# Performance work log

Measured on AMD Instinct MI355X. Metric: run time of the kernel, lower is better.

## Reference

```python
import jax, jax.numpy as jnp
import numpy as np

EPS = 1e-5

def layer_norm(x, g, b):
    mu = jnp.mean(x, axis=-1, keepdims=True)
    var = jnp.mean(jnp.square(x - mu), axis=-1, keepdims=True)
    return (x - mu) * jax.lax.rsqrt(var + EPS) * g + b

def setup_inputs() -> dict:
    key = jax.random.key(0)
    B, N, IN_D, S, D = 64, 4096, 256, 8, 256
    ks = jax.random.split(key, 20)
    scale = lambda fan_in: 1.0 / np.sqrt(fan_in)
    u = lambda k, shape, s: jax.random.uniform(k, shape, jnp.float32, -s, s)
    return {
        "inputs": jax.random.normal(ks[0], (B, N, IN_D), jnp.float32),
        "noise": jax.random.normal(ks[1], (B, S, D), jnp.float32),
        "slots_mu": jax.random.normal(ks[2], (1, S, D), jnp.float32),
        "slots_sigma": jnp.ones((1, S, D), jnp.float32) * 0.1,
        "Wq": u(ks[3], (D, D), scale(D)), "bq": u(ks[4], (D,), scale(D)),
        "Wk": u(ks[5], (D, IN_D), scale(IN_D)), "bk": u(ks[6], (D,), scale(IN_D)),
        "Wv": u(ks[7], (D, IN_D), scale(IN_D)), "bv": u(ks[8], (D,), scale(IN_D)),
        "W_ih": u(ks[9], (3 * D, D), scale(D)), "b_ih": u(ks[10], (3 * D,), scale(D)),
        "W_hh": u(ks[11], (3 * D, D), scale(D)), "b_hh": u(ks[12], (3 * D,), scale(D)),
        "W1": u(ks[13], (D, D), scale(D)), "b1": u(ks[14], (D,), scale(D)),
        "W2": u(ks[15], (D, D), scale(D)), "b2": u(ks[16], (D,), scale(D)),
        "ln_slots_g": jnp.ones((D,), jnp.float32), "ln_slots_b": jnp.zeros((D,), jnp.float32),
        "ln_mlp_g": jnp.ones((D,), jnp.float32), "ln_mlp_b": jnp.zeros((D,), jnp.float32),
    }

def gru_cell(x, h, W_ih, b_ih, W_hh, b_hh):
    # PyTorch GRUCell: gates ordered (reset, update, new)
    gi = x @ W_ih.T + b_ih  # [B*S, 3D]
    gh = h @ W_hh.T + b_hh
    i_r, i_z, i_n = jnp.split(gi, 3, axis=-1)
    h_r, h_z, h_n = jnp.split(gh, 3, axis=-1)
    r = jax.nn.sigmoid(i_r + h_r)
    z = jax.nn.sigmoid(i_z + h_z)
    n = jnp.tanh(i_n + r * h_n)
    return (1.0 - z) * n + z * h

def reference(inputs, noise, slots_mu, slots_sigma, Wq, bq, Wk, bk, Wv, bv,
              W_ih, b_ih, W_hh, b_hh, W1, b1, W2, b2,
              ln_slots_g, ln_slots_b, ln_mlp_g, ln_mlp_b):
    B, N, _ = inputs.shape
    _, S, D = noise.shape
    num_iterations = 3
    slots = slots_mu + slots_sigma * noise  # [B, S, D]
    # k, v are loop-invariant; hoist the big GEMMs out of the iteration loop
    k = jnp.einsum('bnd,ed->bne', inputs, Wk) + bk  # [B, N, D]
    v = jnp.einsum('bnd,ed->bne', inputs, Wv) + bv  # [B, N, D]
    inv_sqrt_d = 1.0 / np.sqrt(D)
    for _ in range(num_iterations):
        slots_prev = slots
        q = layer_norm(slots, ln_slots_g, ln_slots_b) @ Wq.T + bq  # [B, S, D]
        attn_logits = jnp.einsum('bsd,bnd->bsn', q, k) * inv_sqrt_d
        attn = jax.nn.softmax(attn_logits, axis=-1)  # softmax over inputs (dim=-1)
        updates = jnp.einsum('bsn,bnd->bsd', attn, v)  # [B, S, D]
        h_new = gru_cell(updates.reshape(-1, D), slots_prev.reshape(-1, D),
                         W_ih, b_ih, W_hh, b_hh).reshape(B, S, D)
        slots = slots_prev + h_new  # residual around GRU (as in source)
        hidden = jax.nn.relu(layer_norm(slots, ln_mlp_g, ln_mlp_b) @ W1.T + b1)
        slots = slots + (hidden @ W2.T + b2)
    return slots
```

## Files before the change

### kernel.cpp

```cpp
#include <hip/hip_runtime.h>


constexpr int Bn = 64;
constexpr int Nn = 4096;
constexpr int Dd = 256;
constexpr int Ss = 8;
constexpr int CH = 16;
constexpr float EPSF = 1e-5f;

#define DEV __device__ __forceinline__

using short8 = __attribute__((ext_vector_type(8))) short;
using f32x4 = __attribute__((ext_vector_type(4))) float;
union U8 { short8 s; uint4 u; };

DEV unsigned bfpack2(float lo, float hi) {
  unsigned ul = __float_as_uint(lo), uh = __float_as_uint(hi);
  ul = (ul + 0x7FFFu + ((ul >> 16) & 1u)) >> 16;
  uh = (uh + 0x7FFFu + ((uh >> 16) & 1u)) & 0xFFFF0000u;
  return ul | uh;
}
DEV unsigned short bf16r(float x) {
  unsigned u = __float_as_uint(x);
  u = (u + 0x7FFFu + ((u >> 16) & 1u)) >> 16;
  return (unsigned short)u;
}
DEV float rsum32(float v) {
  v += __shfl_xor(v, 1); v += __shfl_xor(v, 2); v += __shfl_xor(v, 4);
  v += __shfl_xor(v, 8); v += __shfl_xor(v, 16);
  return v;
}
DEV float sigm(float x) { return 1.f / (1.f + __expf(-x)); }

template <int NK>
DEV void load_af(short8* a, const unsigned short* base, int lda, int m16, int quad) {
  const unsigned short* p = base + m16 * lda + quad * 8;
#pragma unroll
  for (int kk = 0; kk < NK; ++kk) a[kk] = *(const short8*)(p + kk * 32);
}
template <int NK>
DEV f32x4 gemm_tile(const short8* a, const unsigned short* wr, float binit) {
  f32x4 acc = {binit, binit, binit, binit};
#pragma unroll
  for (int kk = 0; kk < NK; ++kk) {
    short8 b = *(const short8*)(wr + kk * 32);
    acc = __builtin_amdgcn_mfma_f32_16x16x32_bf16(a[kk], b, acc, 0, 0, 0);
  }
  return acc;
}

DEV void ln_row8(const float* x, const float* g, const float* b, int d0,
                 unsigned short* dst) {
  float s = x[0] + x[1] + x[2] + x[3] + x[4] + x[5] + x[6] + x[7];
  float mu = rsum32(s) * (1.f / 256.f);
  float q = 0.f;
#pragma unroll
  for (int j = 0; j < 8; ++j) { float d = x[j] - mu; q += d * d; }
  float rs = rsqrtf(rsum32(q) * (1.f / 256.f) + EPSF);
  float o[8];
#pragma unroll
  for (int j = 0; j < 8; ++j) o[j] = (x[j] - mu) * rs * g[d0 + j] + b[d0 + j];
  uint4 w;
  w.x = bfpack2(o[0], o[1]); w.y = bfpack2(o[2], o[3]);
  w.z = bfpack2(o[4], o[5]); w.w = bfpack2(o[6], o[7]);
  *(uint4*)dst = w;
}

__global__ __launch_bounds__(256) void k_wqk(const float* __restrict__ Wq,
                                             const float* __restrict__ Wk,
                                             const float* __restrict__ bq,
                                             unsigned short* __restrict__ Wqk_b,
                                             float* __restrict__ bqk) {
  int tid = threadIdx.x, c = blockIdx.x;
  if (c < 256) {
    float acc = 0.f;
    for (int e = 0; e < 256; ++e) acc += Wq[e * 256 + tid] * Wk[e * 256 + c];
    Wqk_b[c * 256 + tid] = bf16r(acc);
  } else {
    float acc = 0.f;
    for (int e = 0; e < 256; ++e) acc += bq[e] * Wk[e * 256 + tid];
    bqk[tid] = acc;
  }
}

__global__ __launch_bounds__(256) void k_conv(
    const float* __restrict__ Wv, const float* __restrict__ Wih,
    const float* __restrict__ Whh, const float* __restrict__ W1,
    const float* __restrict__ W2,
    const float* __restrict__ bih, const float* __restrict__ bhh,
    unsigned* Wv_b, unsigned* Wzr_b, unsigned* Win_b, unsigned* Whn_b,
    unsigned* W1_b, unsigned* W2_b, float* bzr) {
  if (blockIdx.x >= 1152) {
    int i = (blockIdx.x - 1152) * 256 + threadIdx.x;
    if (i < 512) bzr[i] = bih[i] + bhh[i];
    return;
  }
  int p = blockIdx.x * 256 + threadIdx.x;
  const float* src; unsigned* dst;
  if (p < 32768) { src = Wv + 2 * p; dst = Wv_b + p; }
  else if (p < 163840) {
    int q = p - 32768, row = q >> 8, col = (q & 255) * 2;
    src = (col < 256) ? (Wih + row * 256 + col) : (Whh + row * 256 + col - 256);
    dst = Wzr_b + q;
  }
  else if (p < 196608) { int q = p - 163840; src = Wih + 512 * 256 + 2 * q; dst = Win_b + q; }
  else if (p < 229376) { int q = p - 196608; src = Whh + 512 * 256 + 2 * q; dst = Whn_b + q; }
  else if (p < 262144) { int q = p - 229376; src = W1 + 2 * q; dst = W1_b + q; }
  else { int q = p - 262144; src = W2 + 2 * q; dst = W2_b + q; }
  dst[0] = bfpack2(src[0], src[1]);
}

__global__ __launch_bounds__(512) void k_qk0(const float* __restrict__ noise,
                                             const float* __restrict__ s_mu,
                                             const float* __restrict__ s_sg,
                                             const float* __restrict__ gsl,
                                             const float* __restrict__ bsl,
                                             const unsigned short* __restrict__ Wqk_b,
                                             const float* __restrict__ bqk,
                                             float* __restrict__ slots,
                                             float* __restrict__ qk) {
  __shared__ __align__(16) unsigned short lnb[16 * 264];
  const int tid = threadIdx.x, bb = blockIdx.x;
  const int lane = tid & 63, wave = tid >> 6;
  const int m16 = lane & 15, quad = lane >> 4;
  const int row = tid >> 5, l32 = tid & 31, d0 = l32 * 8;
  {
    const int grow = bb * 16 + row;
    const int sidx = (grow & 7) * 256 + d0;
    const float* np = noise + (size_t)grow * 256 + d0;
    float4 n0 = *(const float4*)np, n1 = *(const float4*)(np + 4);
    float4 m0 = *(const float4*)(s_mu + sidx), m1 = *(const float4*)(s_mu + sidx + 4);
    float4 g0 = *(const float4*)(s_sg + sidx), g1 = *(const float4*)(s_sg + sidx + 4);
    float x[8] = {m0.x + g0.x * n0.x, m0.y + g0.y * n0.y,
                  m0.z + g0.z * n0.z, m0.w + g0.w * n0.w,
                  m1.x + g1.x * n1.x, m1.y + g1.y * n1.y,
                  m1.z + g1.z * n1.z, m1.w + g1.w * n1.w};
    float* sp_ = slots + (size_t)grow * 256 + d0;
    float4 o0, o1;
    o0.x = x[0]; o0.y = x[1]; o0.z = x[2]; o0.w = x[3];
    o1.x = x[4]; o1.y = x[5]; o1.z = x[6]; o1.w = x[7];
    *(float4*)sp_ = o0; *(float4*)(sp_ + 4) = o1;
    ln_row8(x, gsl, bsl, d0, lnb + row * 264 + d0);
  }
  __syncthreads();
  short8 a8[8];
  load_af<8>(a8, lnb, 264, m16, quad);
#pragma unroll
  for (int i = 0; i < 2; ++i) {
    int t = wave + 8 * i;
    f32x4 acc = gemm_tile<8>(a8, Wqk_b + (size_t)(t * 16 + m16) * 256 + quad * 8,
                             bqk[t * 16 + m16]);
#pragma unroll
    for (int r = 0; r < 4; ++r)
      qk[(size_t)(bb * 16 + quad * 4 + r) * 256 + t * 16 + m16] = acc[r] * 0.0625f;
  }
}

template <bool FIRST>
DEV void ld_chunk(const float* __restrict__ xin, unsigned* __restrict__ xbf,
                  size_t nbase, int tid, uint4* pr) {
#pragma unroll
  for (int i = 0; i < 8; ++i) {
    int flat = i * 256 + tid, n = flat >> 5, od = flat & 31;
    if (FIRST) {
      const float4* src = (const float4*)(xin + (nbase + n) * 256 + od * 8);
      float4 v0 = src[0], v1 = src[1];
      uint4 o;
      o.x = bfpack2(v0.x, v0.y); o.y = bfpack2(v0.z, v0.w);
      o.z = bfpack2(v1.x, v1.y); o.w = bfpack2(v1.z, v1.w);
      ((uint4*)xbf)[(nbase + n) * 32 + od] = o;
      pr[i] = o;
    } else {
      pr[i] = ((const uint4*)xbf)[(nbase + n) * 32 + od];
    }
  }
}

template <bool FIRST>
__global__ __launch_bounds__(256) void k_attn(const float* __restrict__ xin,
                                              unsigned* __restrict__ xbf,
                                              const float* __restrict__ qk,
                                              float* __restrict__ pl,
                                              float* __restrict__ pu) {
  __shared__ __align__(16) unsigned xt[128 * 65];
  __shared__ __align__(16) unsigned pp[32 * 17];
  __shared__ __align__(16) float lred[4][16];
  const int tid = threadIdx.x;
  const int lane = tid & 63, wave = tid >> 6;
  const int m16 = lane & 15, quad = lane >> 4;
  const int c = blockIdx.x, b = blockIdx.y;
  const int pb = (b * CH + c) * 8;
  const unsigned psel = (m16 & 1) ? 0x07060302u : 0x05040100u;

  short8 aq[8];
  {
    const float* qrow = qk + (size_t)(b * 8 + (m16 & 7)) * 256 + quad * 8;
#pragma unroll
    for (int kk = 0; kk < 8; ++kk) {
      U8 f;
      float4 q0 = *(const float4*)(qrow + kk * 32);
      float4 q1 = *(const float4*)(qrow + kk * 32 + 4);
      f.u.x = bfpack2(q0.x, q0.y); f.u.y = bfpack2(q0.z, q0.w);
      f.u.z = bfpack2(q1.x, q1.y); f.u.w = bfpack2(q1.z, q1.w);
      if (m16 >= 8) { f.u.x = 0u; f.u.y = 0u; f.u.z = 0u; f.u.w = 0u; }
      aq[kk] = f.s;
    }
  }
  float lacc[4] = {0.f, 0.f, 0.f, 0.f};
  f32x4 acc[4];
#pragma unroll
  for (int t = 0; t < 4; ++t) acc[t] = (f32x4){0.f, 0.f, 0.f, 0.f};
  const int d0w = wave * 64;

  uint4 pr[8];
  const size_t nb0 = (size_t)b * Nn + (size_t)c * 256;
  ld_chunk<FIRST>(xin, xbf, nb0, tid, pr);

  for (int ch = 0; ch < 4; ++ch) {
#pragma unroll
    for (int i = 0; i < 8; ++i) {
      int flat = i * 256 + tid, n = flat >> 5, od = flat & 31, rb = od * 4;
      xt[(rb + 0) * 65 + n] = pr[i].x;
      xt[(rb + 1) * 65 + n] = pr[i].y;
      xt[(rb + 2) * 65 + n] = pr[i].z;
      xt[(rb + 3) * 65 + n] = pr[i].w;
    }
    __syncthreads();
    if (ch + 1 < 4)
      ld_chunk<FIRST>(xin, xbf, nb0 + (size_t)(ch + 1) * 64, tid, pr);
    {
      const int nt = wave;
      f32x4 pacc = (f32x4){0.f, 0.f, 0.f, 0.f};
#pragma unroll
      for (int kk = 0; kk < 8; ++kk) {
        int base = (kk * 16 + quad * 4) * 65 + nt * 16 + m16;
        U8 bf;
        bf.u.x = xt[base]; bf.u.y = xt[base + 65];
        bf.u.z = xt[base + 130]; bf.u.w = xt[base + 195];
        pacc = __builtin_amdgcn_mfma_f32_16x16x32_bf16(aq[kk], bf.s, pacc, 0, 0, 0);
      }
      const int xrow = nt * 16 + m16;
      unsigned short* pps = (unsigned short*)pp;
#pragma unroll
      for (int r = 0; r < 4; ++r) {
        float p = __expf(pacc[r]);
        lacc[r] += p;
        pps[((xrow >> 1) * 17 + quad * 4 + r) * 2 + (xrow & 1)] = bf16r(p);
      }
    }
    __syncthreads();
#pragma unroll
    for (int nh = 0; nh < 2; ++nh) {
      U8 bp;
      bp.u.x = pp[(nh * 16 + quad * 4 + 0) * 17 + m16];
      bp.u.y = pp[(nh * 16 + quad * 4 + 1) * 17 + m16];
      bp.u.z = pp[(nh * 16 + quad * 4 + 2) * 17 + m16];
      bp.u.w = pp[(nh * 16 + quad * 4 + 3) * 17 + m16];
#pragma unroll
      for (int t = 0; t < 4; ++t) {
        int d = d0w + t * 16 + m16;
        const unsigned* xr = xt + (d >> 1) * 65 + nh * 32 + quad * 8;
        unsigned u0 = xr[0], u1 = xr[1], u2 = xr[2], u3 = xr[3];
        unsigned u4 = xr[4], u5 = xr[5], u6 = xr[6], u7 = xr[7];
        U8 af;
        af.u.x = __builtin_amdgcn_perm(u1, u0, psel);
        af.u.y = __builtin_amdgcn_perm(u3, u2, psel);
        af.u.z = __builtin_amdgcn_perm(u5, u4, psel);
        af.u.w = __builtin_amdgcn_perm(u7, u6, psel);
        acc[t] = __builtin_amdgcn_mfma_f32_16x16x32_bf16(af.s, bp.s, acc[t], 0, 0, 0);
      }
    }
    __syncthreads();
  }
  if (m16 < 8) {
#pragma unroll
    for (int t = 0; t < 4; ++t)
#pragma unroll
      for (int r = 0; r < 4; ++r)
        pu[(size_t)(pb + m16) * 256 + d0w + t * 16 + quad * 4 + r] = acc[t][r];
  }
  {
#pragma unroll
    for (int r = 0; r < 4; ++r) {
      float v = lacc[r];
      v += __shfl_xor(v, 1); v += __shfl_xor(v, 2);
      v += __shfl_xor(v, 4); v += __shfl_xor(v, 8);
      if (m16 == 0) lred[wave][quad * 4 + r] = v;
    }
  }
  __syncthreads();
  if (tid < 8)
    pl[pb + tid] = lred[0][tid] + lred[1][tid] + lred[2][tid] + lred[3][tid];
}

__global__ __launch_bounds__(512) void k_upd(
    const float* __restrict__ pl, const float* __restrict__ pu,
    const unsigned short* __restrict__ Wv_b, const float* __restrict__ bv,
    const unsigned short* __restrict__ Wzr_b, const float* __restrict__ bzr,
    const unsigned short* __restrict__ Win_b, const float* __restrict__ bin,
    const unsigned short* __restrict__ Whn_b, const float* __restrict__ bhn,
    const unsigned short* __restrict__ W1_b, const float* __restrict__ b1,
    const unsigned short* __restrict__ W2_b, const float* __restrict__ b2,
    const float* __restrict__ gml, const float* __restrict__ bml,
    const float* __restrict__ gsl, const float* __restrict__ bsl,
    const unsigned short* __restrict__ Wqk_b, const float* __restrict__ bqk,
    float* __restrict__ slots, float* __restrict__ qk, float* __restrict__ dout) {
  __shared__ __align__(16) unsigned short cat[16 * 520];
  __shared__ __align__(16) float sp[16 * 260];
  __shared__ __align__(16) float s1[16 * 260];
  __shared__ __align__(16) unsigned short lnb[16 * 264];
  const int tid = threadIdx.x, bb = blockIdx.x;
  const int lane = tid & 63, wave = tid >> 6;
  const int m16 = lane & 15, quad = lane >> 4;
  const int row = tid >> 5, l32 = tid & 31, d0 = l32 * 8;
  const int bat = 2 * bb + (row >> 3), sl = row & 7;
  {
    float L = 0.f;
#pragma unroll
    for (int cc = 0; cc < 16; ++cc) L += pl[(bat * 16 + cc) * 8 + sl];
    float li = 1.f / L;
    float a[8] = {0.f, 0.f, 0.f, 0.f, 0.f, 0.f, 0.f, 0.f};
    for (int cc = 0; cc < 16; ++cc) {
      const float* pp_ = pu + ((size_t)(bat * 16 + cc) * 8 + sl) * 256 + d0;
      float4 v0 = *(const float4*)pp_, v1 = *(const float4*)(pp_ + 4);
      a[0] += v0.x; a[1] += v0.y; a[2] += v0.z; a[3] += v0.w;
      a[4] += v1.x; a[5] += v1.y; a[6] += v1.z; a[7] += v1.w;
    }
    uint4 o;
    o.x = bfpack2(a[0] * li, a[1] * li); o.y = bfpack2(a[2] * li, a[3] * li);
    o.z = bfpack2(a[4] * li, a[5] * li); o.w = bfpack2(a[6] * li, a[7] * li);
    *(uint4*)(cat + row * 520 + d0) = o;
    const float* sp_ = slots + (size_t)(bb * 16 + row) * 256 + d0;
    float4 h0 = *(const float4*)sp_, h1 = *(const float4*)(sp_ + 4);
    *(float4*)(sp + row * 260 + d0) = h0;
    *(float4*)(sp + row * 260 + d0 + 4) = h1;
    uint4 hb;
    hb.x = bfpack2(h0.x, h0.y); hb.y = bfpack2(h0.z, h0.w);
    hb.z = bfpack2(h1.x, h1.y); hb.w = bfpack2(h1.z, h1.w);
    *(uint4*)(cat + row * 520 + 256 + d0) = hb;
  }
  __syncthreads();
  short8 afr[16];
  load_af<8>(afr, cat, 520, m16, quad);
  f32x4 accv[2];
#pragma unroll
  for (int i = 0; i < 2; ++i) {
    int t = wave + 8 * i;
    accv[i] = gemm_tile<8>(afr, Wv_b + (size_t)(t * 16 + m16) * 256 + quad * 8,
                           bv[t * 16 + m16]);
  }
  __syncthreads();
#pragma unroll
  for (int i = 0; i < 2; ++i) {
    int t = wave + 8 * i;
#pragma unroll
    for (int r = 0; r < 4; ++r)
      cat[(quad * 4 + r) * 520 + t * 16 + m16] = bf16r(accv[i][r]);
  }
  __syncthreads();
  load_af<16>(afr, cat, 520, m16, quad);
  f32x4 rr[2], zz[2];
#pragma unroll
  for (int i = 0; i < 2; ++i) {
    int t = wave + 8 * i;
    f32x4 ar = gemm_tile<16>(afr, Wzr_b + (size_t)(t * 16 + m16) * 512 + quad * 8,
                             bzr[t * 16 + m16]);
    f32x4 az = gemm_tile<16>(afr, Wzr_b + (size_t)((t + 16) * 16 + m16) * 512 + quad * 8,
                             bzr[(t + 16) * 16 + m16]);
#pragma unroll
    for (int r = 0; r < 4; ++r) { rr[i][r] = sigm(ar[r]); zz[i][r] = sigm(az[r]); }
  }
#pragma unroll
  for (int i = 0; i < 2; ++i) {
    int t = wave + 8 * i, col = t * 16 + m16;
    f32x4 ain = gemm_tile<8>(afr, Win_b + (size_t)(t * 16 + m16) * 256 + quad * 8,
                             bin[col]);
    f32x4 ahn = gemm_tile<8>(afr + 8, Whn_b + (size_t)(t * 16 + m16) * 256 + quad * 8,
                             bhn[col]);
#pragma unroll
    for (int r = 0; r < 4; ++r) {
      int rw = quad * 4 + r;
      float nin = ain[r] + rr[i][r] * ahn[r];
      float nn = 1.f - 2.f / (__expf(2.f * nin) + 1.f);
      float hpc = sp[rw * 260 + col];
      s1[rw * 260 + col] = hpc + (1.f - zz[i][r]) * nn + zz[i][r] * hpc;
    }
  }
  __syncthreads();
  {
    const float* s1r = s1 + row * 260 + d0;
    float4 v0 = *(const float4*)s1r, v1 = *(const float4*)(s1r + 4);
    float x[8] = {v0.x, v0.y, v0.z, v0.w, v1.x, v1.y, v1.z, v1.w};
    ln_row8(x, gml, bml, d0, lnb + row * 264 + d0);
  }
  __syncthreads();
  load_af<8>(afr, lnb, 264, m16, quad);
#pragma unroll
  for (int i = 0; i < 2; ++i) {
    int t = wave + 8 * i;
    f32x4 acc = gemm_tile<8>(afr, W1_b + (size_t)(t * 16 + m16) * 256 + quad * 8,
                             b1[t * 16 + m16]);
#pragma unroll
    for (int r = 0; r < 4; ++r)
      cat[(quad * 4 + r) * 520 + t * 16 + m16] = bf16r(fmaxf(acc[r], 0.f));
  }
  __syncthreads();
  load_af<8>(afr, cat, 520, m16, quad);
#pragma unroll
  for (int i = 0; i < 2; ++i) {
    int t = wave + 8 * i;
    f32x4 acc = gemm_tile<8>(afr, W2_b + (size_t)(t * 16 + m16) * 256 + quad * 8,
                             b2[t * 16 + m16]);
#pragma unroll
    for (int r = 0; r < 4; ++r) {
      int rw = quad * 4 + r, col = t * 16 + m16;
      float v = acc[r] + s1[rw * 260 + col];
      size_t gi = (size_t)(bb * 16 + rw) * 256 + col;
      slots[gi] = v;
      if (dout) dout[gi] = v;
      sp[rw * 260 + col] = v;
    }
  }
  __syncthreads();
  {
    const float* spr = sp + row * 260 + d0;
    float4 v0 = *(const float4*)spr, v1 = *(const float4*)(spr + 4);
    float x[8] = {v0.x, v0.y, v0.z, v0.w, v1.x, v1.y, v1.z, v1.w};
    ln_row8(x, gsl, bsl, d0, lnb + row * 264 + d0);
  }
  __syncthreads();
  load_af<8>(afr, lnb, 264, m16, quad);
#pragma unroll
  for (int i = 0; i < 2; ++i) {
    int t = wave + 8 * i;
    f32x4 acc = gemm_tile<8>(afr, Wqk_b + (size_t)(t * 16 + m16) * 256 + quad * 8,
                             bqk[t * 16 + m16]);
#pragma unroll
    for (int r = 0; r < 4; ++r)
      qk[(size_t)(bb * 16 + quad * 4 + r) * 256 + t * 16 + m16] = acc[r] * 0.0625f;
  }
}

extern "C" void kernel_launch(void* const* d_in, const int* in_sizes, int n_in,
                              void* d_out, int out_size, void* d_ws, size_t ws_size,
                              hipStream_t stream) {
  const float* inputs = (const float*)d_in[0];
  const float* noise = (const float*)d_in[1];
  const float* s_mu = (const float*)d_in[2];
  const float* s_sg = (const float*)d_in[3];
  const float* Wq = (const float*)d_in[4];
  const float* bq = (const float*)d_in[5];
  const float* Wk = (const float*)d_in[6];
  const float* Wv = (const float*)d_in[8];
  const float* bv = (const float*)d_in[9];
  const float* Wih = (const float*)d_in[10];
  const float* bih = (const float*)d_in[11];
  const float* Whh = (const float*)d_in[12];
  const float* bhh = (const float*)d_in[13];
  const float* W1 = (const float*)d_in[14];
  const float* b1 = (const float*)d_in[15];
  const float* W2 = (const float*)d_in[16];
  const float* b2 = (const float*)d_in[17];
  const float* gsl = (const float*)d_in[18];
  const float* bsl = (const float*)d_in[19];
  const float* gml = (const float*)d_in[20];
  const float* bml = (const float*)d_in[21];
  float* out = (float*)d_out;

  char* wsb = (char*)d_ws;
  unsigned* xbf = (unsigned*)wsb;
  float* fp = (float*)(wsb + (size_t)Bn * Nn * Dd * 2);
  float* slots = fp; fp += Bn * Ss * Dd;
  float* qk = fp;    fp += Bn * Ss * Dd;
  float* bqk = fp;   fp += Dd;
  float* pl = fp;    fp += Bn * CH * Ss;
  float* pu = fp;    fp += Bn * CH * Ss * Dd;
  float* bzr = fp;   fp += 512;
  unsigned short* wb = (unsigned short*)fp;
  unsigned short* Wv_b = wb;  wb += 65536;
  unsigned short* Wzr_b = wb; wb += 262144;
  unsigned short* Win_b = wb; wb += 65536;
  unsigned short* Whn_b = wb; wb += 65536;
  unsigned short* W1_b = wb;  wb += 65536;
  unsigned short* W2_b = wb;  wb += 65536;
  unsigned short* Wqk_b = wb; wb += 65536;
  (void)in_sizes; (void)n_in; (void)out_size; (void)ws_size;

  k_wqk<<<dim3(257), dim3(256), 0, stream>>>(Wq, Wk, bq, Wqk_b, bqk);
  k_conv<<<dim3(1154), dim3(256), 0, stream>>>(
      Wv, Wih, Whh, W1, W2, bih, bhh, (unsigned*)Wv_b, (unsigned*)Wzr_b,
      (unsigned*)Win_b, (unsigned*)Whn_b, (unsigned*)W1_b, (unsigned*)W2_b, bzr);
  k_qk0<<<dim3(32), dim3(512), 0, stream>>>(noise, s_mu, s_sg, gsl, bsl, Wqk_b, bqk,
                                            slots, qk);
  for (int it = 0; it < 3; ++it) {
    if (it == 0)
      k_attn<true><<<dim3(CH, Bn), dim3(256), 0, stream>>>(inputs, xbf, qk, pl, pu);
    else
      k_attn<false><<<dim3(CH, Bn), dim3(256), 0, stream>>>(nullptr, xbf, qk, pl, pu);
    k_upd<<<dim3(32), dim3(512), 0, stream>>>(
        pl, pu, Wv_b, bv, Wzr_b, bzr, Win_b, bih + 512, Whn_b, bhh + 512, W1_b, b1,
        W2_b, b2, gml, bml, gsl, bsl, Wqk_b, bqk, slots, qk, (it == 2) ? out : nullptr);
  }
}
```

Measured before the change: 686.5 us.

## Fuse slot update into attention kernel via last-block atomic counter

Merges the two weight-prep kernels into one launch, and folds the per-iteration slot-update kernel into the attention kernel. Each attention block increments a per-batch-pair atomic counter, and the last of the 32 blocks for that pair runs the GRU/MLP/query update with 256 threads. This removes three kernel launches and their boundaries, but the update now runs serialized on a single straggler block per pair with half the threads, and it adds fences and atomics.

```diff
diff --git a/kernel.cpp b/kernel.cpp
--- a/kernel.cpp
+++ b/kernel.cpp
@@ -66,48 +66,333 @@
   *(uint4*)dst = w;
 }
 
-__global__ __launch_bounds__(256) void k_wqk(const float* __restrict__ Wq,
-                                             const float* __restrict__ Wk,
-                                             const float* __restrict__ bq,
-                                             unsigned short* __restrict__ Wqk_b,
-                                             float* __restrict__ bqk) {
-  int tid = threadIdx.x, c = blockIdx.x;
-  if (c < 256) {
+
+template <bool FIRST>
+DEV void ld_chunk_t(const float* __restrict__ xin, unsigned* __restrict__ xbf,
+                    size_t nbase, int tid, uint4* pr) {
+#pragma unroll
+  for (int i = 0; i < 8; ++i) {
+    int flat = i * 256 + tid, n = flat >> 5, od = flat & 31;
+    if (FIRST) {
+      const float4* src = (const float4*)(xin + (nbase + n) * 256 + od * 8);
+      float4 v0 = src[0], v1 = src[1];
+      uint4 o;
+      o.x = bfpack2(v0.x, v0.y); o.y = bfpack2(v0.z, v0.w);
+      o.z = bfpack2(v1.x, v1.y); o.w = bfpack2(v1.z, v1.w);
+      ((uint4*)xbf)[(nbase + n) * 32 + od] = o;
+      pr[i] = o;
+    } else {
+      pr[i] = ((const uint4*)xbf)[(nbase + n) * 32 + od];
+    }
+  }
+}
+
+template <bool FIRST>
+DEV void attn_unit(const float* __restrict__ xin, unsigned* __restrict__ xbf,
+                   const float* __restrict__ qk, float* __restrict__ pl,
+                   float* __restrict__ pu, unsigned* xt, unsigned* pp,
+                   float (*lred)[16], int u, int tid) {
+  const int lane = tid & 63, wave = tid >> 6;
+  const int m16 = lane & 15, quad = lane >> 4;
+  const int b = u >> 4, c = u & 15;
+  const int pb = u * 8;
+  const unsigned psel = (m16 & 1) ? 0x07060302u : 0x05040100u;
+
+  short8 aq[8];
+  {
+    const float* qrow = qk + (size_t)(b * 8 + (m16 & 7)) * 256 + quad * 8;
+#pragma unroll
+    for (int kk = 0; kk < 8; ++kk) {
+      U8 f;
+      float4 q0 = *(const float4*)(qrow + kk * 32);
+      float4 q1 = *(const float4*)(qrow + kk * 32 + 4);
+      f.u.x = bfpack2(q0.x, q0.y); f.u.y = bfpack2(q0.z, q0.w);
+      f.u.z = bfpack2(q1.x, q1.y); f.u.w = bfpack2(q1.z, q1.w);
+      if (m16 >= 8) { f.u.x = 0u; f.u.y = 0u; f.u.z = 0u; f.u.w = 0u; }
+      aq[kk] = f.s;
+    }
+  }
+  float lacc[4] = {0.f, 0.f, 0.f, 0.f};
+  f32x4 acc[4];
+#pragma unroll
+  for (int t = 0; t < 4; ++t) acc[t] = (f32x4){0.f, 0.f, 0.f, 0.f};
+  const int d0w = wave * 64;
+
+  uint4 pr[8];
+  const size_t nb0 = (size_t)b * Nn + (size_t)c * 256;
+  ld_chunk_t<FIRST>(xin, xbf, nb0, tid, pr);
+
+  for (int ch = 0; ch < 4; ++ch) {
+#pragma unroll
+    for (int i = 0; i < 8; ++i) {
+      int flat = i * 256 + tid, n = flat >> 5, od = flat & 31, rb = od * 4;
+      xt[(rb + 0) * 65 + n] = pr[i].x;
+      xt[(rb + 1) * 65 + n] = pr[i].y;
+      xt[(rb + 2) * 65 + n] = pr[i].z;
+      xt[(rb + 3) * 65 + n] = pr[i].w;
+    }
+    __syncthreads();
+    if (ch + 1 < 4)
+      ld_chunk_t<FIRST>(xin, xbf, nb0 + (size_t)(ch + 1) * 64, tid, pr);
+    {
+      const int nt = wave;
+      f32x4 pacc = (f32x4){0.f, 0.f, 0.f, 0.f};
+#pragma unroll
+      for (int kk = 0; kk < 8; ++kk) {
+        int base = (kk * 16 + quad * 4) * 65 + nt * 16 + m16;
+        U8 bf;
+        bf.u.x = xt[base]; bf.u.y = xt[base + 65];
+        bf.u.z = xt[base + 130]; bf.u.w = xt[base + 195];
+        pacc = __builtin_amdgcn_mfma_f32_16x16x32_bf16(aq[kk], bf.s, pacc, 0, 0, 0);
+      }
+      const int xrow = nt * 16 + m16;
+      unsigned short* pps = (unsigned short*)pp;
+#pragma unroll
+      for (int r = 0; r < 4; ++r) {
+        float p = __expf(pacc[r]);
+        lacc[r] += p;
+        pps[((xrow >> 1) * 17 + quad * 4 + r) * 2 + (xrow & 1)] = bf16r(p);
+      }
+    }
+    __syncthreads();
+#pragma unroll
+    for (int nh = 0; nh < 2; ++nh) {
+      U8 bp;
+      bp.u.x = pp[(nh * 16 + quad * 4 + 0) * 17 + m16];
+      bp.u.y = pp[(nh * 16 + quad * 4 + 1) * 17 + m16];
+      bp.u.z = pp[(nh * 16 + quad * 4 + 2) * 17 + m16];
+      bp.u.w = pp[(nh * 16 + quad * 4 + 3) * 17 + m16];
+#pragma unroll
+      for (int t = 0; t < 4; ++t) {
+        int d = d0w + t * 16 + m16;
+        const unsigned* xr = xt + (d >> 1) * 65 + nh * 32 + quad * 8;
+        unsigned u0 = xr[0], u1 = xr[1], u2 = xr[2], u3 = xr[3];
+        unsigned u4 = xr[4], u5 = xr[5], u6 = xr[6], u7 = xr[7];
+        U8 af;
+        af.u.x = __builtin_amdgcn_perm(u1, u0, psel);
+        af.u.y = __builtin_amdgcn_perm(u3, u2, psel);
+        af.u.z = __builtin_amdgcn_perm(u5, u4, psel);
+        af.u.w = __builtin_amdgcn_perm(u7, u6, psel);
+        acc[t] = __builtin_amdgcn_mfma_f32_16x16x32_bf16(af.s, bp.s, acc[t], 0, 0, 0);
+      }
+    }
+    __syncthreads();
+  }
+  if (m16 < 8) {
+#pragma unroll
+    for (int t = 0; t < 4; ++t)
+#pragma unroll
+      for (int r = 0; r < 4; ++r)
+        pu[(size_t)(pb + m16) * 256 + d0w + t * 16 + quad * 4 + r] = acc[t][r];
+  }
+#pragma unroll
+  for (int r = 0; r < 4; ++r) {
+    float v = lacc[r];
+    v += __shfl_xor(v, 1); v += __shfl_xor(v, 2);
+    v += __shfl_xor(v, 4); v += __shfl_xor(v, 8);
+    if (m16 == 0) lred[wave][quad * 4 + r] = v;
+  }
+  __syncthreads();
+  if (tid < 8)
+    pl[pb + tid] = lred[0][tid] + lred[1][tid] + lred[2][tid] + lred[3][tid];
+}
+
+DEV void upd_body256(
+    const float* __restrict__ pl, const float* __restrict__ pu,
+    const unsigned short* __restrict__ Wv_b, const float* __restrict__ bv,
+    const unsigned short* __restrict__ Wzr_b, const float* __restrict__ bzr,
+    const unsigned short* __restrict__ Win_b, const float* __restrict__ bin,
+    const unsigned short* __restrict__ Whn_b, const float* __restrict__ bhn,
+    const unsigned short* __restrict__ W1_b, const float* __restrict__ b1,
+    const unsigned short* __restrict__ W2_b, const float* __restrict__ b2,
+    const float* __restrict__ gml, const float* __restrict__ bml,
+    const float* __restrict__ gsl, const float* __restrict__ bsl,
+    const unsigned short* __restrict__ Wqk_b, const float* __restrict__ bqk,
+    float* __restrict__ slots, float* __restrict__ qk, float* __restrict__ dout,
+    unsigned short* cat, float* sp, int bb, int tid) {
+  unsigned short* lnbp = cat + 256;
+  const int lane = tid & 63, wave4 = tid >> 6;
+  const int m16 = lane & 15, quad = lane >> 4;
+  const int row8 = tid >> 5, l32 = tid & 31, d0 = l32 * 8;
+#pragma unroll
+  for (int r2 = 0; r2 < 2; ++r2) {
+    const int row = row8 + 8 * r2;
+    const int bat = 2 * bb + (row >> 3), sl = row & 7;
+    float L = 0.f;
+#pragma unroll
+    for (int cc = 0; cc < 16; ++cc) L += pl[(bat * 16 + cc) * 8 + sl];
+    float li = 1.f / L;
+    float a[8] = {0.f, 0.f, 0.f, 0.f, 0.f, 0.f, 0.f, 0.f};
+    for (int cc = 0; cc < 16; ++cc) {
+      const float* pp_ = pu + ((size_t)(bat * 16 + cc) * 8 + sl) * 256 + d0;
+      float4 v0 = *(const float4*)pp_, v1 = *(const float4*)(pp_ + 4);
+      a[0] += v0.x; a[1] += v0.y; a[2] += v0.z; a[3] += v0.w;
+      a[4] += v1.x; a[5] += v1.y; a[6] += v1.z; a[7] += v1.w;
+    }
+    uint4 o;
+    o.x = bfpack2(a[0] * li, a[1] * li); o.y = bfpack2(a[2] * li, a[3] * li);
+    o.z = bfpack2(a[4] * li, a[5] * li); o.w = bfpack2(a[6] * li, a[7] * li);
+    *(uint4*)(cat + row * 520 + d0) = o;
+    const float* sp_ = slots + (size_t)(bb * 16 + row) * 256 + d0;
+    float4 h0 = *(const float4*)sp_, h1 = *(const float4*)(sp_ + 4);
+    *(float4*)(sp + row * 260 + d0) = h0;
+    *(float4*)(sp + row * 260 + d0 + 4) = h1;
+    uint4 hb;
+    hb.x = bfpack2(h0.x, h0.y); hb.y = bfpack2(h0.z, h0.w);
+    hb.z = bfpack2(h1.x, h1.y); hb.w = bfpack2(h1.z, h1.w);
+    *(uint4*)(cat + row * 520 + 256 + d0) = hb;
+  }
+  __syncthreads();
+  short8 afr[16];
+  load_af<8>(afr, cat, 520, m16, quad);
+  f32x4 accv[4];
+#pragma unroll
+  for (int i = 0; i < 4; ++i) {
+    int t = wave4 + 4 * i;
+    accv[i] = gemm_tile<8>(afr, Wv_b + (size_t)(t * 16 + m16) * 256 + quad * 8,
+                           bv[t * 16 + m16]);
+  }
+  __syncthreads();
+#pragma unroll
+  for (int i = 0; i < 4; ++i) {
+    int t = wave4 + 4 * i;
+#pragma unroll
+    for (int r = 0; r < 4; ++r)
+      cat[(quad * 4 + r) * 520 + t * 16 + m16] = bf16r(accv[i][r]);
+  }
+  __syncthreads();
+  load_af<16>(afr, cat, 520, m16, quad);
+#pragma unroll
+  for (int i = 0; i < 4; ++i) {
+    int t = wave4 + 4 * i, col = t * 16 + m16;
+    f32x4 ar = gemm_tile<16>(afr, Wzr_b + (size_t)(t * 16 + m16) * 512 + quad * 8,
+                             bzr[t * 16 + m16]);
+    f32x4 az = gemm_tile<16>(afr, Wzr_b + (size_t)((t + 16) * 16 + m16) * 512 + quad * 8,
+                             bzr[(t + 16) * 16 + m16]);
+    f32x4 ain = gemm_tile<8>(afr, Win_b + (size_t)(t * 16 + m16) * 256 + quad * 8,
+                             bin[col]);
+    f32x4 ahn = gemm_tile<8>(afr + 8, Whn_b + (size_t)(t * 16 + m16) * 256 + quad * 8,
+                             bhn[col]);
+#pragma unroll
+    for (int r = 0; r < 4; ++r) {
+      int rw = quad * 4 + r;
+      float rrv = sigm(ar[r]), zzv = sigm(az[r]);
+      float nin = ain[r] + rrv * ahn[r];
+      float nn = 1.f - 2.f / (__expf(2.f * nin) + 1.f);
+      float hpc = sp[rw * 260 + col];
+      sp[rw * 260 + col] = hpc + (1.f - zzv) * nn + zzv * hpc;
+    }
+  }
+  __syncthreads();
+#pragma unroll
+  for (int r2 = 0; r2 < 2; ++r2) {
+    int row = row8 + 8 * r2;
+    const float* s1r = sp + row * 260 + d0;
+    float4 v0 = *(const float4*)s1r, v1 = *(const float4*)(s1r + 4);
+    float x[8] = {v0.x, v0.y, v0.z, v0.w, v1.x, v1.y, v1.z, v1.w};
+    ln_row8(x, gml, bml, d0, lnbp + row * 520 + d0);
+  }
+  __syncthreads();
+  load_af<8>(afr, lnbp, 520, m16, quad);
+#pragma unroll
+  for (int i = 0; i < 4; ++i) {
+    int t = wave4 + 4 * i;
+    f32x4 acc = gemm_tile<8>(afr, W1_b + (size_t)(t * 16 + m16) * 256 + quad * 8,
+                             b1[t * 16 + m16]);
+#pragma unroll
+    for (int r = 0; r < 4; ++r)
+      cat[(quad * 4 + r) * 520 + t * 16 + m16] = bf16r(fmaxf(acc[r], 0.f));
+  }
+  __syncthreads();
+  load_af<8>(afr, cat, 520, m16, quad);
+#pragma unroll
+  for (int i = 0; i < 4; ++i) {
+    int t = wave4 + 4 * i;
+    f32x4 acc = gemm_tile<8>(afr, W2_b + (size_t)(t * 16 + m16) * 256 + quad * 8,
+                             b2[t * 16 + m16]);
+#pragma unroll
+    for (int r = 0; r < 4; ++r) {
+      int rw = quad * 4 + r, col = t * 16 + m16;
+      float v = acc[r] + sp[rw * 260 + col];
+      size_t gi = (size_t)(bb * 16 + rw) * 256 + col;
+      slots[gi] = v;
+      if (dout) dout[gi] = v;
+      sp[rw * 260 + col] = v;
+    }
+  }
+  __syncthreads();
+#pragma unroll
+  for (int r2 = 0; r2 < 2; ++r2) {
+    int row = row8 + 8 * r2;
+    const float* spr = sp + row * 260 + d0;
+    float4 v0 = *(const float4*)spr, v1 = *(const float4*)(spr + 4);
+    float x[8] = {v0.x, v0.y, v0.z, v0.w, v1.x, v1.y, v1.z, v1.w};
+    ln_row8(x, gsl, bsl, d0, lnbp + row * 520 + d0);
+  }
+  __syncthreads();
+  load_af<8>(afr, lnbp, 520, m16, quad);
+#pragma unroll
+  for (int i = 0; i < 4; ++i) {
+    int t = wave4 + 4 * i;
+    f32x4 acc = gemm_tile<8>(afr, Wqk_b + (size_t)(t * 16 + m16) * 256 + quad * 8,
+                             bqk[t * 16 + m16]);
+#pragma unroll
+    for (int r = 0; r < 4; ++r)
+      qk[(size_t)(bb * 16 + quad * 4 + r) * 256 + t * 16 + m16] = acc[r] * 0.0625f;
+  }
+}
+
+DEV void prep_unit(int u, int tid,
+                   const float* Wq, const float* Wk, const float* bq,
+                   unsigned short* Wqk_b, float* bqk,
+                   const float* Wv, const float* Wih, const float* Whh,
+                   const float* W1, const float* W2,
+                   const float* bih, const float* bhh,
+                   unsigned* Wv_b, unsigned* Wzr_b, unsigned* Win_b, unsigned* Whn_b,
+                   unsigned* W1_b, unsigned* W2_b, float* bzr) {
+  if (u < 256) {
     float acc = 0.f;
-    for (int e = 0; e < 256; ++e) acc += Wq[e * 256 + tid] * Wk[e * 256 + c];
-    Wqk_b[c * 256 + tid] = bf16r(acc);
-  } else {
+    for (int e = 0; e < 256; ++e) acc += Wq[e * 256 + tid] * Wk[e * 256 + u];
+    Wqk_b[u * 256 + tid] = bf16r(acc);
+  } else if (u == 256) {
     float acc = 0.f;
     for (int e = 0; e < 256; ++e) acc += bq[e] * Wk[e * 256 + tid];
     bqk[tid] = acc;
-  }
-}
-
-__global__ __launch_bounds__(256) void k_conv(
-    const float* __restrict__ Wv, const float* __restrict__ Wih,
-    const float* __restrict__ Whh, const float* __restrict__ W1,
-    const float* __restrict__ W2,
+  } else {
+    int cu = u - 257;
+    if (cu >= 1152) {
+      int i = (cu - 1152) * 256 + tid;
+      if (i < 512) bzr[i] = bih[i] + bhh[i];
+      return;
+    }
+    int p = cu * 256 + tid;
+    const float* src; unsigned* dst;
+    if (p < 32768) { src = Wv + 2 * p; dst = Wv_b + p; }
+    else if (p < 163840) {
+      int q = p - 32768, row = q >> 8, col = (q & 255) * 2;
+      src = (col < 256) ? (Wih + row * 256 + col) : (Whh + row * 256 + col - 256);
+      dst = Wzr_b + q;
+    }
+    else if (p < 196608) { int q = p - 163840; src = Wih + 512 * 256 + 2 * q; dst = Win_b + q; }
+    else if (p < 229376) { int q = p - 196608; src = Whh + 512 * 256 + 2 * q; dst = Whn_b + q; }
+    else if (p < 262144) { int q = p - 229376; src = W1 + 2 * q; dst = W1_b + q; }
+    else { int q = p - 262144; src = W2 + 2 * q; dst = W2_b + q; }
+    dst[0] = bfpack2(src[0], src[1]);
+  }
+}
+
+
+__global__ __launch_bounds__(256) void k_prep(
+    const float* __restrict__ Wq, const float* __restrict__ Wk,
+    const float* __restrict__ bq, unsigned short* __restrict__ Wqk_b,
+    float* __restrict__ bqk, const float* __restrict__ Wv,
+    const float* __restrict__ Wih, const float* __restrict__ Whh,
+    const float* __restrict__ W1, const float* __restrict__ W2,
     const float* __restrict__ bih, const float* __restrict__ bhh,
     unsigned* Wv_b, unsigned* Wzr_b, unsigned* Win_b, unsigned* Whn_b,
     unsigned* W1_b, unsigned* W2_b, float* bzr) {
-  if (blockIdx.x >= 1152) {
-    int i = (blockIdx.x - 1152) * 256 + threadIdx.x;
-    if (i < 512) bzr[i] = bih[i] + bhh[i];
-    return;
-  }
-  int p = blockIdx.x * 256 + threadIdx.x;
-  const float* src; unsigned* dst;
-  if (p < 32768) { src = Wv + 2 * p; dst = Wv_b + p; }
-  else if (p < 163840) {
-    int q = p - 32768, row = q >> 8, col = (q & 255) * 2;
-    src = (col < 256) ? (Wih + row * 256 + col) : (Whh + row * 256 + col - 256);
-    dst = Wzr_b + q;
-  }
-  else if (p < 196608) { int q = p - 163840; src = Wih + 512 * 256 + 2 * q; dst = Win_b + q; }
-  else if (p < 229376) { int q = p - 196608; src = Whh + 512 * 256 + 2 * q; dst = Whn_b + q; }
-  else if (p < 262144) { int q = p - 229376; src = W1 + 2 * q; dst = W1_b + q; }
-  else { int q = p - 262144; src = W2 + 2 * q; dst = W2_b + q; }
-  dst[0] = bfpack2(src[0], src[1]);
+  prep_unit(blockIdx.x, threadIdx.x, Wq, Wk, bq, Wqk_b, bqk, Wv, Wih, Whh, W1, W2,
+            bih, bhh, Wv_b, Wzr_b, Win_b, Whn_b, W1_b, W2_b, bzr);
 }
 
 __global__ __launch_bounds__(512) void k_qk0(const float* __restrict__ noise,
@@ -118,9 +403,11 @@
                                              const unsigned short* __restrict__ Wqk_b,
                                              const float* __restrict__ bqk,
                                              float* __restrict__ slots,
-                                             float* __restrict__ qk) {
+                                             float* __restrict__ qk,
+                                             int* __restrict__ cnt) {
   __shared__ __align__(16) unsigned short lnb[16 * 264];
   const int tid = threadIdx.x, bb = blockIdx.x;
+  if (bb == 0 && tid < 32) cnt[tid] = 0;
   const int lane = tid & 63, wave = tid >> 6;
   const int m16 = lane & 15, quad = lane >> 4;
   const int row = tid >> 5, l32 = tid & 31, d0 = l32 * 8;
@@ -156,288 +443,42 @@
   }
 }
 
-template <bool FIRST>
-DEV void ld_chunk(const float* __restrict__ xin, unsigned* __restrict__ xbf,
-                  size_t nbase, int tid, uint4* pr) {
-#pragma unroll
-  for (int i = 0; i < 8; ++i) {
-    int flat = i * 256 + tid, n = flat >> 5, od = flat & 31;
-    if (FIRST) {
-      const float4* src = (const float4*)(xin + (nbase + n) * 256 + od * 8);
-      float4 v0 = src[0], v1 = src[1];
-      uint4 o;
-      o.x = bfpack2(v0.x, v0.y); o.y = bfpack2(v0.z, v0.w);
-      o.z = bfpack2(v1.x, v1.y); o.w = bfpack2(v1.z, v1.w);
-      ((uint4*)xbf)[(nbase + n) * 32 + od] = o;
-      pr[i] = o;
-    } else {
-      pr[i] = ((const uint4*)xbf)[(nbase + n) * 32 + od];
-    }
-  }
-}
-
-template <bool FIRST>
-__global__ __launch_bounds__(256) void k_attn(const float* __restrict__ xin,
-                                              unsigned* __restrict__ xbf,
-                                              const float* __restrict__ qk,
-                                              float* __restrict__ pl,
-                                              float* __restrict__ pu) {
-  __shared__ __align__(16) unsigned xt[128 * 65];
-  __shared__ __align__(16) unsigned pp[32 * 17];
-  __shared__ __align__(16) float lred[4][16];
+struct IterArgs {
+  const float* xin;
+  unsigned* xbf;
+  float *qk, *pl, *pu;
+  int* cnt;
+  const unsigned short *Wv_b, *Wzr_b, *Win_b, *Whn_b, *W1_b, *W2_b, *Wqk_b;
+  const float *bv, *bzr, *bin, *bhn, *b1, *b2, *gml, *bml, *gsl, *bsl, *bqk;
+  float *slots, *out;
+};
+
+template <int IT>
+__global__ __launch_bounds__(256) void k_attn_f(IterArgs a) {
+  __shared__ __align__(16) union SMU {
+    struct { unsigned xt[128 * 65]; unsigned pp[32 * 17]; float lred[4][16]; } at;
+    struct { unsigned short cat[16 * 520]; float sp[16 * 260]; } up;
+  } sm;
+  __shared__ int win;
   const int tid = threadIdx.x;
-  const int lane = tid & 63, wave = tid >> 6;
-  const int m16 = lane & 15, quad = lane >> 4;
-  const int c = blockIdx.x, b = blockIdx.y;
-  const int pb = (b * CH + c) * 8;
-  const unsigned psel = (m16 & 1) ? 0x07060302u : 0x05040100u;
-
-  short8 aq[8];
-  {
-    const float* qrow = qk + (size_t)(b * 8 + (m16 & 7)) * 256 + quad * 8;
-#pragma unroll
-    for (int kk = 0; kk < 8; ++kk) {
-      U8 f;
-      float4 q0 = *(const float4*)(qrow + kk * 32);
-      float4 q1 = *(const float4*)(qrow + kk * 32 + 4);
-      f.u.x = bfpack2(q0.x, q0.y); f.u.y = bfpack2(q0.z, q0.w);
-      f.u.z = bfpack2(q1.x, q1.y); f.u.w = bfpack2(q1.z, q1.w);
-      if (m16 >= 8) { f.u.x = 0u; f.u.y = 0u; f.u.z = 0u; f.u.w = 0u; }
-      aq[kk] = f.s;
-    }
-  }
-  float lacc[4] = {0.f, 0.f, 0.f, 0.f};
-  f32x4 acc[4];
-#pragma unroll
-  for (int t = 0; t < 4; ++t) acc[t] = (f32x4){0.f, 0.f, 0.f, 0.f};
-  const int d0w = wave * 64;
-
-  uint4 pr[8];
-  const size_t nb0 = (size_t)b * Nn + (size_t)c * 256;
-  ld_chunk<FIRST>(xin, xbf, nb0, tid, pr);
-
-  for (int ch = 0; ch < 4; ++ch) {
-#pragma unroll
-    for (int i = 0; i < 8; ++i) {
-      int flat = i * 256 + tid, n = flat >> 5, od = flat & 31, rb = od * 4;
-      xt[(rb + 0) * 65 + n] = pr[i].x;
-      xt[(rb + 1) * 65 + n] = pr[i].y;
-      xt[(rb + 2) * 65 + n] = pr[i].z;
-      xt[(rb + 3) * 65 + n] = pr[i].w;
-    }
-    __syncthreads();
-    if (ch + 1 < 4)
-      ld_chunk<FIRST>(xin, xbf, nb0 + (size_t)(ch + 1) * 64, tid, pr);
-    {
-      const int nt = wave;
-      f32x4 pacc = (f32x4){0.f, 0.f, 0.f, 0.f};
-#pragma unroll
-      for (int kk = 0; kk < 8; ++kk) {
-        int base = (kk * 16 + quad * 4) * 65 + nt * 16 + m16;
-        U8 bf;
-        bf.u.x = xt[base]; bf.u.y = xt[base + 65];
-        bf.u.z = xt[base + 130]; bf.u.w = xt[base + 195];
-        pacc = __builtin_amdgcn_mfma_f32_16x16x32_bf16(aq[kk], bf.s, pacc, 0, 0, 0);
-      }
-      const int xrow = nt * 16 + m16;
-      unsigned short* pps = (unsigned short*)pp;
-#pragma unroll
-      for (int r = 0; r < 4; ++r) {
-        float p = __expf(pacc[r]);
-        lacc[r] += p;
-        pps[((xrow >> 1) * 17 + quad * 4 + r) * 2 + (xrow & 1)] = bf16r(p);
-      }
-    }
-    __syncthreads();
-#pragma unroll
-    for (int nh = 0; nh < 2; ++nh) {
-      U8 bp;
-      bp.u.x = pp[(nh * 16 + quad * 4 + 0) * 17 + m16];
-      bp.u.y = pp[(nh * 16 + quad * 4 + 1) * 17 + m16];
-      bp.u.z = pp[(nh * 16 + quad * 4 + 2) * 17 + m16];
-      bp.u.w = pp[(nh * 16 + quad * 4 + 3) * 17 + m16];
-#pragma unroll
-      for (int t = 0; t < 4; ++t) {
-        int d = d0w + t * 16 + m16;
-        const unsigned* xr = xt + (d >> 1) * 65 + nh * 32 + quad * 8;
-        unsigned u0 = xr[0], u1 = xr[1], u2 = xr[2], u3 = xr[3];
-        unsigned u4 = xr[4], u5 = xr[5], u6 = xr[6], u7 = xr[7];
-        U8 af;
-        af.u.x = __builtin_amdgcn_perm(u1, u0, psel);
-        af.u.y = __builtin_amdgcn_perm(u3, u2, psel);
-        af.u.z = __builtin_amdgcn_perm(u5, u4, psel);
-        af.u.w = __builtin_amdgcn_perm(u7, u6, psel);
-        acc[t] = __builtin_amdgcn_mfma_f32_16x16x32_bf16(af.s, bp.s, acc[t], 0, 0, 0);
-      }
-    }
-    __syncthreads();
-  }
-  if (m16 < 8) {
-#pragma unroll
-    for (int t = 0; t < 4; ++t)
-#pragma unroll
-      for (int r = 0; r < 4; ++r)
-        pu[(size_t)(pb + m16) * 256 + d0w + t * 16 + quad * 4 + r] = acc[t][r];
-  }
-  {
-#pragma unroll
-    for (int r = 0; r < 4; ++r) {
-      float v = lacc[r];
-      v += __shfl_xor(v, 1); v += __shfl_xor(v, 2);
-      v += __shfl_xor(v, 4); v += __shfl_xor(v, 8);
-      if (m16 == 0) lred[wave][quad * 4 + r] = v;
-    }
-  }
-  __syncthreads();
-  if (tid < 8)
-    pl[pb + tid] = lred[0][tid] + lred[1][tid] + lred[2][tid] + lred[3][tid];
-}
-
-__global__ __launch_bounds__(512) void k_upd(
-    const float* __restrict__ pl, const float* __restrict__ pu,
-    const unsigned short* __restrict__ Wv_b, const float* __restrict__ bv,
-    const unsigned short* __restrict__ Wzr_b, const float* __restrict__ bzr,
-    const unsigned short* __restrict__ Win_b, const float* __restrict__ bin,
-    const unsigned short* __restrict__ Whn_b, const float* __restrict__ bhn,
-    const unsigned short* __restrict__ W1_b, const float* __restrict__ b1,
-    const unsigned short* __restrict__ W2_b, const float* __restrict__ b2,
-    const float* __restrict__ gml, const float* __restrict__ bml,
-    const float* __restrict__ gsl, const float* __restrict__ bsl,
-    const unsigned short* __restrict__ Wqk_b, const float* __restrict__ bqk,
-    float* __restrict__ slots, float* __restrict__ qk, float* __restrict__ dout) {
-  __shared__ __align__(16) unsigned short cat[16 * 520];
-  __shared__ __align__(16) float sp[16 * 260];
-  __shared__ __align__(16) float s1[16 * 260];
-  __shared__ __align__(16) unsigned short lnb[16 * 264];
-  const int tid = threadIdx.x, bb = blockIdx.x;
-  const int lane = tid & 63, wave = tid >> 6;
-  const int m16 = lane & 15, quad = lane >> 4;
-  const int row = tid >> 5, l32 = tid & 31, d0 = l32 * 8;
-  const int bat = 2 * bb + (row >> 3), sl = row & 7;
-  {
-    float L = 0.f;
-#pragma unroll
-    for (int cc = 0; cc < 16; ++cc) L += pl[(bat * 16 + cc) * 8 + sl];
-    float li = 1.f / L;
-    float a[8] = {0.f, 0.f, 0.f, 0.f, 0.f, 0.f, 0.f, 0.f};
-    for (int cc = 0; cc < 16; ++cc) {
-      const float* pp_ = pu + ((size_t)(bat * 16 + cc) * 8 + sl) * 256 + d0;
-      float4 v0 = *(const float4*)pp_, v1 = *(const float4*)(pp_ + 4);
-      a[0] += v0.x; a[1] += v0.y; a[2] += v0.z; a[3] += v0.w;
-      a[4] += v1.x; a[5] += v1.y; a[6] += v1.z; a[7] += v1.w;
-    }
-    uint4 o;
-    o.x = bfpack2(a[0] * li, a[1] * li); o.y = bfpack2(a[2] * li, a[3] * li);
-    o.z = bfpack2(a[4] * li, a[5] * li); o.w = bfpack2(a[6] * li, a[7] * li);
-    *(uint4*)(cat + row * 520 + d0) = o;
-    const float* sp_ = slots + (size_t)(bb * 16 + row) * 256 + d0;
-    float4 h0 = *(const float4*)sp_, h1 = *(const float4*)(sp_ + 4);
-    *(float4*)(sp + row * 260 + d0) = h0;
-    *(float4*)(sp + row * 260 + d0 + 4) = h1;
-    uint4 hb;
-    hb.x = bfpack2(h0.x, h0.y); hb.y = bfpack2(h0.z, h0.w);
-    hb.z = bfpack2(h1.x, h1.y); hb.w = bfpack2(h1.z, h1.w);
-    *(uint4*)(cat + row * 520 + 256 + d0) = hb;
-  }
-  __syncthreads();
-  short8 afr[16];
-  load_af<8>(afr, cat, 520, m16, quad);
-  f32x4 accv[2];
-#pragma unroll
-  for (int i = 0; i < 2; ++i) {
-    int t = wave + 8 * i;
-    accv[i] = gemm_tile<8>(afr, Wv_b + (size_t)(t * 16 + m16) * 256 + quad * 8,
-                           bv[t * 16 + m16]);
-  }
-  __syncthreads();
-#pragma unroll
-  for (int i = 0; i < 2; ++i) {
-    int t = wave + 8 * i;
-#pragma unroll
-    for (int r = 0; r < 4; ++r)
-      cat[(quad * 4 + r) * 520 + t * 16 + m16] = bf16r(accv[i][r]);
-  }
-  __syncthreads();
-  load_af<16>(afr, cat, 520, m16, quad);
-  f32x4 rr[2], zz[2];
-#pragma unroll
-  for (int i = 0; i < 2; ++i) {
-    int t = wave + 8 * i;
-    f32x4 ar = gemm_tile<16>(afr, Wzr_b + (size_t)(t * 16 + m16) * 512 + quad * 8,
-                             bzr[t * 16 + m16]);
-    f32x4 az = gemm_tile<16>(afr, Wzr_b + (size_t)((t + 16) * 16 + m16) * 512 + quad * 8,
-                             bzr[(t + 16) * 16 + m16]);
-#pragma unroll
-    for (int r = 0; r < 4; ++r) { rr[i][r] = sigm(ar[r]); zz[i][r] = sigm(az[r]); }
-  }
-#pragma unroll
-  for (int i = 0; i < 2; ++i) {
-    int t = wave + 8 * i, col = t * 16 + m16;
-    f32x4 ain = gemm_tile<8>(afr, Win_b + (size_t)(t * 16 + m16) * 256 + quad * 8,
-                             bin[col]);
-    f32x4 ahn = gemm_tile<8>(afr + 8, Whn_b + (size_t)(t * 16 + m16) * 256 + quad * 8,
-                             bhn[col]);
-#pragma unroll
-    for (int r = 0; r < 4; ++r) {
-      int rw = quad * 4 + r;
-      float nin = ain[r] + rr[i][r] * ahn[r];
-      float nn = 1.f - 2.f / (__expf(2.f * nin) + 1.f);
-      float hpc = sp[rw * 260 + col];
-      s1[rw * 260 + col] = hpc + (1.f - zz[i][r]) * nn + zz[i][r] * hpc;
-    }
-  }
-  __syncthreads();
-  {
-    const float* s1r = s1 + row * 260 + d0;
-    float4 v0 = *(const float4*)s1r, v1 = *(const float4*)(s1r + 4);
-    float x[8] = {v0.x, v0.y, v0.z, v0.w, v1.x, v1.y, v1.z, v1.w};
-    ln_row8(x, gml, bml, d0, lnb + row * 264 + d0);
-  }
-  __syncthreads();
-  load_af<8>(afr, lnb, 264, m16, quad);
-#pragma unroll
-  for (int i = 0; i < 2; ++i) {
-    int t = wave + 8 * i;
-    f32x4 acc = gemm_tile<8>(afr, W1_b + (size_t)(t * 16 + m16) * 256 + quad * 8,
-                             b1[t * 16 + m16]);
-#pragma unroll
-    for (int r = 0; r < 4; ++r)
-      cat[(quad * 4 + r) * 520 + t * 16 + m16] = bf16r(fmaxf(acc[r], 0.f));
-  }
-  __syncthreads();
-  load_af<8>(afr, cat, 520, m16, quad);
-#pragma unroll
-  for (int i = 0; i < 2; ++i) {
-    int t = wave + 8 * i;
-    f32x4 acc = gemm_tile<8>(afr, W2_b + (size_t)(t * 16 + m16) * 256 + quad * 8,
-                             b2[t * 16 + m16]);
-#pragma unroll
-    for (int r = 0; r < 4; ++r) {
-      int rw = quad * 4 + r, col = t * 16 + m16;
-      float v = acc[r] + s1[rw * 260 + col];
-      size_t gi = (size_t)(bb * 16 + rw) * 256 + col;
-      slots[gi] = v;
-      if (dout) dout[gi] = v;
-      sp[rw * 260 + col] = v;
-    }
-  }
-  __syncthreads();
-  {
-    const float* spr = sp + row * 260 + d0;
-    float4 v0 = *(const float4*)spr, v1 = *(const float4*)(spr + 4);
-    float x[8] = {v0.x, v0.y, v0.z, v0.w, v1.x, v1.y, v1.z, v1.w};
-    ln_row8(x, gsl, bsl, d0, lnb + row * 264 + d0);
-  }
-  __syncthreads();
-  load_af<8>(afr, lnb, 264, m16, quad);
-#pragma unroll
-  for (int i = 0; i < 2; ++i) {
-    int t = wave + 8 * i;
-    f32x4 acc = gemm_tile<8>(afr, Wqk_b + (size_t)(t * 16 + m16) * 256 + quad * 8,
-                             bqk[t * 16 + m16]);
-#pragma unroll
-    for (int r = 0; r < 4; ++r)
-      qk[(size_t)(bb * 16 + quad * 4 + r) * 256 + t * 16 + m16] = acc[r] * 0.0625f;
+  const int u = (int)blockIdx.y * CH + (int)blockIdx.x;
+  const int bb = u >> 5;
+
+  attn_unit<IT == 0>(a.xin, a.xbf, a.qk, a.pl, a.pu, sm.at.xt, sm.at.pp, sm.at.lred,
+                     u, tid);
+  __syncthreads();
+  if (tid == 0) {
+    __threadfence();
+    int old = atomicAdd(&a.cnt[bb], 1);
+    win = (old == IT * 32 + 31) ? 1 : 0;
+    if (win) __threadfence();
+  }
+  __syncthreads();
+  if (win) {
+    upd_body256(a.pl, a.pu, a.Wv_b, a.bv, a.Wzr_b, a.bzr, a.Win_b, a.bin, a.Whn_b,
+                a.bhn, a.W1_b, a.b1, a.W2_b, a.b2, a.gml, a.bml, a.gsl, a.bsl,
+                a.Wqk_b, a.bqk, a.slots, a.qk, (IT == 2) ? a.out : nullptr,
+                sm.up.cat, sm.up.sp, bb, tid);
   }
 }
 
@@ -476,6 +517,7 @@
   float* pl = fp;    fp += Bn * CH * Ss;
   float* pu = fp;    fp += Bn * CH * Ss * Dd;
   float* bzr = fp;   fp += 512;
+  int* cnt = (int*)fp; fp += 32;
   unsigned short* wb = (unsigned short*)fp;
   unsigned short* Wv_b = wb;  wb += 65536;
   unsigned short* Wzr_b = wb; wb += 262144;
@@ -486,19 +528,20 @@
   unsigned short* Wqk_b = wb; wb += 65536;
   (void)in_sizes; (void)n_in; (void)out_size; (void)ws_size;
 
-  k_wqk<<<dim3(257), dim3(256), 0, stream>>>(Wq, Wk, bq, Wqk_b, bqk);
-  k_conv<<<dim3(1154), dim3(256), 0, stream>>>(
-      Wv, Wih, Whh, W1, W2, bih, bhh, (unsigned*)Wv_b, (unsigned*)Wzr_b,
-      (unsigned*)Win_b, (unsigned*)Whn_b, (unsigned*)W1_b, (unsigned*)W2_b, bzr);
+  k_prep<<<dim3(1411), dim3(256), 0, stream>>>(
+      Wq, Wk, bq, Wqk_b, bqk, Wv, Wih, Whh, W1, W2, bih, bhh, (unsigned*)Wv_b,
+      (unsigned*)Wzr_b, (unsigned*)Win_b, (unsigned*)Whn_b, (unsigned*)W1_b,
+      (unsigned*)W2_b, bzr);
   k_qk0<<<dim3(32), dim3(512), 0, stream>>>(noise, s_mu, s_sg, gsl, bsl, Wqk_b, bqk,
-                                            slots, qk);
-  for (int it = 0; it < 3; ++it) {
-    if (it == 0)
-      k_attn<true><<<dim3(CH, Bn), dim3(256), 0, stream>>>(inputs, xbf, qk, pl, pu);
-    else
-      k_attn<false><<<dim3(CH, Bn), dim3(256), 0, stream>>>(nullptr, xbf, qk, pl, pu);
-    k_upd<<<dim3(32), dim3(512), 0, stream>>>(
-        pl, pu, Wv_b, bv, Wzr_b, bzr, Win_b, bih + 512, Whn_b, bhh + 512, W1_b, b1,
-        W2_b, b2, gml, bml, gsl, bsl, Wqk_b, bqk, slots, qk, (it == 2) ? out : nullptr);
-  }
-}
+                                            slots, qk, cnt);
+  IterArgs a;
+  a.xin = inputs; a.xbf = xbf; a.qk = qk; a.pl = pl; a.pu = pu; a.cnt = cnt;
+  a.Wv_b = Wv_b; a.Wzr_b = Wzr_b; a.Win_b = Win_b; a.Whn_b = Whn_b;
+  a.W1_b = W1_b; a.W2_b = W2_b; a.Wqk_b = Wqk_b;
+  a.bv = bv; a.bzr = bzr; a.bin = bih + 512; a.bhn = bhh + 512;
+  a.b1 = b1; a.b2 = b2; a.gml = gml; a.bml = bml; a.gsl = gsl; a.bsl = bsl;
+  a.bqk = bqk; a.slots = slots; a.out = out;
+  k_attn_f<0><<<dim3(CH, Bn), dim3(256), 0, stream>>>(a);
+  k_attn_f<1><<<dim3(CH, Bn), dim3(256), 0, stream>>>(a);
+  k_attn_f<2><<<dim3(CH, Bn), dim3(256), 0, stream>>>(a);
+}
```

Measured after the change: 911.3 us. 32.7% more time.
